# Optimization experiments

Measured on AMD Instinct MI355X. Metric: run time of the kernel, lower is better.

The kernel has to match this reference:

```python
import jax, jax.numpy as jnp
import numpy as np

ALPHA = 1.702  # gpt-oss gated-activation alpha
LIMIT = 7.0    # gpt-oss clamp limit
E, H, I = 8, 1024, 2048
B, S = 2, 2048


def setup_inputs() -> dict:
    key = jax.random.key(0)
    ks = jax.random.split(key, 6)
    return {
        "hidden_states": jax.random.normal(ks[0], (B, S, H), dtype=jnp.float32),
        "routing_weights": jax.random.uniform(ks[1], (B * S, E), dtype=jnp.float32),
        "gate_up_proj": jax.random.normal(ks[2], (E, H, 2 * I), dtype=jnp.float32) * 0.02,
        "gate_up_proj_bias": jax.random.normal(ks[3], (E, 2 * I), dtype=jnp.float32) * 0.02,
        "down_proj": jax.random.normal(ks[4], (E, I, H), dtype=jnp.float32) * 0.02,
        "down_proj_bias": jax.random.normal(ks[5], (E, H), dtype=jnp.float32) * 0.02,
    }


def reference(hidden_states, routing_weights, gate_up_proj, gate_up_proj_bias,
              down_proj, down_proj_bias):
    b, s, h = hidden_states.shape
    x = hidden_states.reshape(-1, h)  # [T, H]
    # all-experts dense path: [E, T, 2I]
    gate_up = jnp.einsum('th,ehd->etd', x, gate_up_proj) + gate_up_proj_bias[:, None, :]
    gate = gate_up[..., ::2]   # interleaved gate/up as in gpt-oss
    up = gate_up[..., 1::2]
    gate = jnp.minimum(gate, LIMIT)
    up = jnp.clip(up, -LIMIT, LIMIT)
    glu = gate * jax.nn.sigmoid(gate * ALPHA)
    # [E, T, H]
    out_e = jnp.einsum('eti,eih->eth', (up + 1.0) * glu, down_proj) + down_proj_bias[:, None, :]
    # weighted sum over experts with routing weights [T, E]
    out = jnp.einsum('eth,te->th', out_e, routing_weights)
    return out.reshape(b, s, h)
```

## Files before the change

### kernel.cpp

```cpp
#include <hip/hip_runtime.h>
#include <cstdint>

#define E_  8
#define H_  1024
#define I_  2048
#define T_  4096
#define D2_ 4096
#define K2_ 16384

typedef __bf16 bf16x8 __attribute__((ext_vector_type(8)));
typedef float  f32x4  __attribute__((ext_vector_type(4)));

__device__ __forceinline__ unsigned short f2bf(float f) {
  unsigned int u = __float_as_uint(f);
  u += 0x7FFFu + ((u >> 16) & 1u);
  return (unsigned short)(u >> 16);
}

__device__ __forceinline__ void gll16(const void* g, void* l) {
  __builtin_amdgcn_global_load_lds(
      (const __attribute__((address_space(1))) unsigned int*)(uintptr_t)g,
      (__attribute__((address_space(3))) unsigned int*)(uintptr_t)l,
      16, 0, 0);
}

#define BARX()  __builtin_amdgcn_s_barrier()
#define FENCE() __builtin_amdgcn_sched_barrier(0)
#define LGK0()  asm volatile("s_waitcnt lgkmcnt(0)" ::: "memory")
#define WVM0()  asm volatile("s_waitcnt vmcnt(0)" ::: "memory")

__global__ void cast_x_kernel(const float* __restrict__ x,
                              unsigned short* __restrict__ xb) {
  const int idx = (blockIdx.x * 256 + threadIdx.x) * 8;
  float4 a = *(const float4*)(x + idx);
  float4 b = *(const float4*)(x + idx + 4);
  unsigned short o[8];
  o[0]=f2bf(a.x); o[1]=f2bf(a.y); o[2]=f2bf(a.z); o[3]=f2bf(a.w);
  o[4]=f2bf(b.x); o[5]=f2bf(b.y); o[6]=f2bf(b.z); o[7]=f2bf(b.w);
  *(uint4*)(xb + idx) = *(const uint4*)o;
}

__global__ void transp_w1_kernel(const float* __restrict__ gup,
                                 unsigned short* __restrict__ w1g,
                                 unsigned short* __restrict__ w1u) {
  __shared__ float tile[64][65];
  const int h0 = blockIdx.x * 64;
  const int d0 = blockIdx.y * 64;
  const int e  = blockIdx.z;
  const int tid = threadIdx.x;
  const int r  = tid >> 4;
  const int c4 = (tid & 15) * 4;
  const float* src = gup + ((size_t)e * H_ + h0) * D2_ + d0;
#pragma unroll
  for (int c = 0; c < 4; ++c) {
    const int row = r + 16 * c;
    float4 v = *(const float4*)(src + (size_t)row * D2_ + c4);
    tile[row][c4+0] = v.x; tile[row][c4+1] = v.y;
    tile[row][c4+2] = v.z; tile[row][c4+3] = v.w;
  }
  __syncthreads();
  const int hl = tid & 63;
  const int jg = tid >> 6;
  const size_t jbase = (size_t)e * I_ + (d0 >> 1);
#pragma unroll
  for (int jj = 0; jj < 8; ++jj) {
    const int jl = jg * 8 + jj;
    w1g[(jbase + jl) * H_ + h0 + hl] = f2bf(tile[hl][2*jl]);
    w1u[(jbase + jl) * H_ + h0 + hl] = f2bf(tile[hl][2*jl+1]);
  }
}

__global__ void transp_w2_kernel(const float* __restrict__ dp,
                                 unsigned short* __restrict__ w2t) {
  __shared__ float tile[64][65];
  const int k0 = blockIdx.x * 64;
  const int h0 = blockIdx.y * 64;
  const int tid = threadIdx.x;
  const int r  = tid >> 4;
  const int c4 = (tid & 15) * 4;
#pragma unroll
  for (int c = 0; c < 4; ++c) {
    const int row = r + 16 * c;
    float4 v = *(const float4*)(dp + (size_t)(k0 + row) * H_ + h0 + c4);
    tile[row][c4+0] = v.x; tile[row][c4+1] = v.y;
    tile[row][c4+2] = v.z; tile[row][c4+3] = v.w;
  }
  __syncthreads();
  const int kl = tid & 63;
  const int hg = tid >> 6;
#pragma unroll
  for (int hh = 0; hh < 16; ++hh) {
    const int hl = hg * 16 + hh;
    w2t[(size_t)(h0 + hl) * K2_ + k0 + kl] = f2bf(tile[kl][hl]);
  }
}


#define NT1 32

#define STA1(B, KT) {                                                         \
  _Pragma("unroll")                                                           \
  for (int ld = 0; ld < 2; ++ld) {                                            \
    const int r = rS + ld*128;                                                \
    gll16(Ag + (size_t)r * H_ + (KT)*32 + sg, &lds[B][r*32 + sl]);            \
  }                                                                           \
  gll16(Gg + (size_t)rS * H_ + (KT)*32 + sg, &lds[B][8192  + rS*32 + sl]);    \
  gll16(Ug + (size_t)rS * H_ + (KT)*32 + sg, &lds[B][12288 + rS*32 + sl]);    \
}
#define LDALL1(B) {                                                           \
  _Pragma("unroll")                                                           \
  for (int m = 0; m < 8; ++m)                                                 \
    av[m] = *(const bf16x8*)&lds[B][(wm*128 + m*16 + arow)*32 + swr];         \
  _Pragma("unroll")                                                           \
  for (int n = 0; n < 2; ++n) {                                               \
    bgv[n] = *(const bf16x8*)&lds[B][8192  + (wn*32 + n*16 + arow)*32 + swr]; \
    buv[n] = *(const bf16x8*)&lds[B][12288 + (wn*32 + n*16 + arow)*32 + swr]; \
  } }
#define MMA1ALL() {                                                           \
  __builtin_amdgcn_s_setprio(1);                                              \
  _Pragma("unroll")                                                           \
  for (int m = 0; m < 8; ++m)                                                 \
  _Pragma("unroll")                                                           \
  for (int n = 0; n < 2; ++n) {                                               \
    accg[m][n] = __builtin_amdgcn_mfma_f32_16x16x32_bf16(av[m], bgv[n], accg[m][n], 0,0,0); \
    accu[m][n] = __builtin_amdgcn_mfma_f32_16x16x32_bf16(av[m], buv[n], accu[m][n], 0,0,0); \
  }                                                                           \
  __builtin_amdgcn_s_setprio(0); }

#define TILE1(B, U) {                                                         \
  if ((U)+1 < NT1) STA1((B)^1, (U)+1);                                        \
  FENCE();                                                                    \
  LDALL1(B);                                                                  \
  MMA1ALL();                                                                  \
  LGK0();                                                                     \
  if ((U)+1 < NT1) WVM0();                                                    \
  BARX();                                                                     \
  FENCE();                                                                    \
}

__global__ __launch_bounds__(512, 2) void gemm1_act_kernel(
    const unsigned short* __restrict__ xb,
    const unsigned short* __restrict__ w1g,
    const unsigned short* __restrict__ w1u,
    const float* __restrict__ gub,
    const float* __restrict__ rw,
    unsigned short* __restrict__ actW)
{
  __shared__ unsigned short lds[2][16384];
  const int tid  = threadIdx.x;
  const int lane = tid & 63;
  const int wv   = tid >> 6;
  const int wm   = wv >> 2;
  const int wn   = wv & 3;

  const int L  = blockIdx.x + 16 * blockIdx.y;
  const int xk = L & 7, xs = L >> 3;
  const int t0 = ((xk >> 1) * 4 + (xs & 3)) * 256;
  const int j0 = ((xk & 1) * 8 + (xs >> 2)) * 128;
  const int e  = blockIdx.z;

  const int arow = lane & 15;
  const int q    = lane >> 4;
  const int swr  = (q ^ ((arow >> 1) & 3)) * 8;
  const int sg   = ((tid & 3) ^ ((tid >> 3) & 3)) * 8;
  const int sl   = (tid & 3) * 8;
  const int rS   = tid >> 2;

  const unsigned short* Ag = xb  + (size_t)t0 * H_;
  const unsigned short* Gg = w1g + ((size_t)e * I_ + j0) * H_;
  const unsigned short* Ug = w1u + ((size_t)e * I_ + j0) * H_;

  const f32x4 zero = {0.f, 0.f, 0.f, 0.f};
  f32x4 accg[8][2], accu[8][2];
#pragma unroll
  for (int m = 0; m < 8; ++m)
#pragma unroll
    for (int n = 0; n < 2; ++n) { accg[m][n] = zero; accu[m][n] = zero; }
  bf16x8 av[8], bgv[2], buv[2];

  STA1(0, 0);
  WVM0(); BARX(); FENCE();

#pragma unroll 1
  for (int t = 0; t < NT1; t += 2) {
    TILE1(0, t);
    TILE1(1, t+1);
  }

  const float* gbE = gub + (size_t)e * D2_;
#pragma unroll
  for (int n = 0; n < 2; ++n) {
    const int j = j0 + wn*32 + n*16 + arow;
    const float2 bgu = *(const float2*)&gbE[2*j];
#pragma unroll
    for (int mf = 0; mf < 8; ++mf) {
#pragma unroll
      for (int ri = 0; ri < 4; ++ri) {
        const int t = t0 + wm*128 + mf*16 + q*4 + ri;
        float g = accg[mf][n][ri] + bgu.x;
        float u = accu[mf][n][ri] + bgu.y;
        g = fminf(g, 7.0f);
        u = fminf(fmaxf(u, -7.0f), 7.0f);
        const float s   = 1.0f / (1.0f + __expf(-1.702f * g));
        const float val = (u + 1.0f) * (g * s) * rw[t * 8 + e];
        actW[(size_t)t * K2_ + e * I_ + j] = f2bf(val);
      }
    }
  }
}


#define STA2(B, HF, KT) {                                                    \
  _Pragma("unroll")                                                           \
  for (int ld = 0; ld < 2; ++ld) {                                            \
    const int r = rA + (HF)*64 + ld*128;                                      \
    gll16(Ag + (size_t)r * K2_ + (KT)*64 + sg, &lds[B][r*64 + sl]);           \
  } }
#define STB2(B, NH, KT) {                                                    \
  _Pragma("unroll")                                                           \
  for (int ld = 0; ld < 2; ++ld) {                                            \
    const int lr = rA + ld*64;                                                \
    const int r  = (lr & 31) + (NH)*32 + ((lr >> 5) << 6);                    \
    gll16(Bgp + (size_t)r * K2_ + (KT)*64 + sg, &lds[B][16384 + r*64 + sl]);  \
  } }
#define LDA2(B, MH) {                                                         \
  _Pragma("unroll")                                                           \
  for (int m = 0; m < 4; ++m) {                                               \
    const int ro = (wm*128 + (MH)*64 + m*16 + arow) * 64;                     \
    av[m][0] = *(const bf16x8*)&lds[B][ro + sw0];                             \
    av[m][1] = *(const bf16x8*)&lds[B][ro + sw1];                             \
  } }
#define LDB2(B, DST, NH) {                                                   \
  _Pragma("unroll")                                                           \
  for (int n = 0; n < 2; ++n) {                                               \
    const int ro = 16384 + (wn*64 + (NH)*32 + n*16 + arow) * 64;              \
    DST[n][0] = *(const bf16x8*)&lds[B][ro + sw0];                            \
    DST[n][1] = *(const bf16x8*)&lds[B][ro + sw1];                            \
  } }
#define MMA2(MH, NH, BV)                                                      \
  __builtin_amdgcn_s_setprio(1);                                              \
  _Pragma("unroll")                                                           \
  for (int m = 0; m < 4; ++m)                                                 \
  _Pragma("unroll")                                                           \
  for (int n = 0; n < 2; ++n) {                                               \
    acc[(MH)*4+m][(NH)*2+n] = __builtin_amdgcn_mfma_f32_16x16x32_bf16(av[m][0], BV[n][0], acc[(MH)*4+m][(NH)*2+n], 0,0,0); \
    acc[(MH)*4+m][(NH)*2+n] = __builtin_amdgcn_mfma_f32_16x16x32_bf16(av[m][1], BV[n][1], acc[(MH)*4+m][(NH)*2+n], 0,0,0); \
  }                                                                           \
  __builtin_amdgcn_s_setprio(0);

#define NT2 64
#define TILE2(B, U) {                                                         \
  if ((U)+1 < NT2) { STA2((B)^1, 0, (U)+1); STA2((B)^1, 1, (U)+1);            \
                     STB2((B)^1, 0, (U)+1); STB2((B)^1, 1, (U)+1); }          \
  FENCE();                                                                    \
  LDA2(B, 0); LDB2(B, bv0, 0); LDB2(B, bv1, 1);                               \
  MMA2(0, 0, bv0); MMA2(0, 1, bv1);                                           \
  LDA2(B, 1);                                                                 \
  MMA2(1, 0, bv0); MMA2(1, 1, bv1);                                           \
  LGK0();                                                                     \
  if ((U)+1 < NT2) WVM0();                                                    \
  BARX();                                                                     \
  FENCE();                                                                    \
}

__global__ __launch_bounds__(512, 2) void gemm2_kernel(
    const unsigned short* __restrict__ actW,
    const unsigned short* __restrict__ w2t,
    float* __restrict__ part)
{
  __shared__ unsigned short lds[2][32768];
  const int tid  = threadIdx.x;
  const int lane = tid & 63;
  const int wv   = tid >> 6;
  const int wm   = wv >> 2;
  const int wn   = wv & 3;

  const int L  = blockIdx.x + 16 * (blockIdx.y + 4 * blockIdx.z);
  const int xk = L & 7, xs = L >> 3;
  const int t0 = ((xk & 1) * 8 + (xs & 7)) * 256;
  const int h0 = (xs >> 3) * 256;
  const int cz = xk >> 1;
  const int c0 = cz * 4096;

  const int arow = lane & 15;
  const int q    = lane >> 4;
  const int sw0  = ((q    ) ^ (arow & 7)) * 8;
  const int sw1  = ((q + 4) ^ (arow & 7)) * 8;
  const int sg   = ((tid & 7) ^ ((tid >> 3) & 7)) * 8;
  const int sl   = (tid & 7) * 8;
  const int rA   = tid >> 3;

  const unsigned short* Ag  = actW + (size_t)t0 * K2_ + c0;
  const unsigned short* Bgp = w2t  + (size_t)h0 * K2_ + c0;

  const f32x4 zero = {0.f, 0.f, 0.f, 0.f};
  f32x4 acc[8][4];
#pragma unroll
  for (int m = 0; m < 8; ++m)
#pragma unroll
    for (int n = 0; n < 4; ++n) acc[m][n] = zero;
  bf16x8 av[4][2], bv0[2][2], bv1[2][2];

  STA2(0, 0, 0); STA2(0, 1, 0); STB2(0, 0, 0); STB2(0, 1, 0);
  WVM0(); BARX(); FENCE();

#pragma unroll 1
  for (int t = 0; t < NT2; t += 2) {
    TILE2(0, t);
    TILE2(1, t+1);
  }

  float* P = part + (size_t)cz * ((size_t)T_ * H_);
#pragma unroll
  for (int mf = 0; mf < 8; ++mf)
#pragma unroll
    for (int nf = 0; nf < 4; ++nf)
#pragma unroll
      for (int ri = 0; ri < 4; ++ri) {
        const int t = t0 + wm*128 + mf*16 + q*4 + ri;
        const int h = h0 + wn*64 + nf*16 + arow;
        P[(size_t)t * H_ + h] = acc[mf][nf][ri];
      }
}

__global__ void reduce_kernel(const float* __restrict__ part,
                              const float* __restrict__ rw,
                              const float* __restrict__ dpb,
                              float* __restrict__ out) {
  const int idx = blockIdx.x * 256 + threadIdx.x;
  const int t  = idx >> 8;
  const int hq = idx & 255;
  const float4* p = (const float4*)part;
  float4 v = p[idx];
  float4 a;
  a = p[idx + 1048576]; v.x += a.x; v.y += a.y; v.z += a.z; v.w += a.w;
  a = p[idx + 2097152]; v.x += a.x; v.y += a.y; v.z += a.z; v.w += a.w;
  a = p[idx + 3145728]; v.x += a.x; v.y += a.y; v.z += a.z; v.w += a.w;
  const float4 w0 = *(const float4*)(rw + t*8);
  const float4 w1 = *(const float4*)(rw + t*8 + 4);
  const float wgt[8] = {w0.x, w0.y, w0.z, w0.w, w1.x, w1.y, w1.z, w1.w};
  const float4* db = (const float4*)dpb;
#pragma unroll
  for (int e2 = 0; e2 < 8; ++e2) {
    float4 b = db[e2*256 + hq];
    v.x += wgt[e2]*b.x; v.y += wgt[e2]*b.y; v.z += wgt[e2]*b.z; v.w += wgt[e2]*b.w;
  }
  ((float4*)out)[idx] = v;
}

extern "C" void kernel_launch(void* const* d_in, const int* in_sizes, int n_in,
                              void* d_out, int out_size, void* d_ws, size_t ws_size,
                              hipStream_t stream) {
  const float* hs  = (const float*)d_in[0];
  const float* rw  = (const float*)d_in[1];
  const float* gup = (const float*)d_in[2];
  const float* gub = (const float*)d_in[3];
  const float* dp  = (const float*)d_in[4];
  const float* dpb = (const float*)d_in[5];
  float* out = (float*)d_out;

  char* ws = (char*)d_ws;
  unsigned short* xb   = (unsigned short*)(ws);
  unsigned short* w1g  = (unsigned short*)(ws + 8388608);
  unsigned short* w1u  = (unsigned short*)(ws + 41943040);
  float*          part = (float*)(ws + 8388608);
  unsigned short* w2t  = (unsigned short*)(ws + 75497472);
  unsigned short* actW = (unsigned short*)(ws + 109051904);

  hipLaunchKernelGGL(cast_x_kernel, dim3((T_ * H_) / 2048), dim3(256), 0, stream, hs, xb);
  hipLaunchKernelGGL(transp_w1_kernel, dim3(H_/64, D2_/64, E_), dim3(256), 0, stream, gup, w1g, w1u);
  hipLaunchKernelGGL(transp_w2_kernel, dim3(K2_/64, H_/64), dim3(256), 0, stream, dp, w2t);
  hipLaunchKernelGGL(gemm1_act_kernel, dim3(T_/256, I_/128, E_), dim3(512), 0, stream,
                     xb, w1g, w1u, gub, rw, actW);
  hipLaunchKernelGGL(gemm2_kernel, dim3(T_/256, H_/256, 4), dim3(512), 0, stream,
                     actW, w2t, part);
  hipLaunchKernelGGL(reduce_kernel, dim3((T_ * H_ / 4) / 256), dim3(256), 0, stream,
                     part, rw, dpb, out);
}
```

Baseline: 470.6 us.

## Deepen both GEMM LDS pipelines to four stages with partial vmcnt waits

Both GEMM kernels now rotate through four LDS buffers, prefetching three K-tiles ahead. They replace the full vmcnt(0)/lgkmcnt(0) drain with partial vmcnt waits, and skip the trailing barrier on the last tile. This is meant to hide more global-load latency behind the MFMA work. GEMM2 also drops its K-tile from 64 to 32 so four stages fit in the same LDS footprint, reusing GEMM1's swizzle. GEMM1's LDS use doubles to 128 KB per block, which likely prevents two blocks per CU despite the launch bounds.

```diff
diff --git a/kernel.cpp b/kernel.cpp
--- a/kernel.cpp
+++ b/kernel.cpp
@@ -26,8 +26,9 @@
 
 #define BARX()  __builtin_amdgcn_s_barrier()
 #define FENCE() __builtin_amdgcn_sched_barrier(0)
-#define LGK0()  asm volatile("s_waitcnt lgkmcnt(0)" ::: "memory")
 #define WVM0()  asm volatile("s_waitcnt vmcnt(0)" ::: "memory")
+#define VM8()   asm volatile("s_waitcnt vmcnt(8)" ::: "memory")
+#define VM4()   asm volatile("s_waitcnt vmcnt(4)" ::: "memory")
 
 __global__ void cast_x_kernel(const float* __restrict__ x,
                               unsigned short* __restrict__ xb) {
@@ -98,7 +99,7 @@
 
 #define NT1 32
 
-#define STA1(B, KT) {                                                         \
+#define STG1ALL(B, KT) {                                                      \
   _Pragma("unroll")                                                           \
   for (int ld = 0; ld < 2; ++ld) {                                            \
     const int r = rS + ld*128;                                                \
@@ -128,14 +129,14 @@
   __builtin_amdgcn_s_setprio(0); }
 
 #define TILE1(B, U) {                                                         \
-  if ((U)+1 < NT1) STA1((B)^1, (U)+1);                                        \
+  if ((U)+3 < NT1) STG1ALL(((B)+3)&3, (U)+3);                                 \
   FENCE();                                                                    \
   LDALL1(B);                                                                  \
   MMA1ALL();                                                                  \
-  LGK0();                                                                     \
-  if ((U)+1 < NT1) WVM0();                                                    \
-  BARX();                                                                     \
-  FENCE();                                                                    \
+  if ((U)+3 < NT1)      { VM8(); }                                            \
+  else if ((U)+2 < NT1) { VM4(); }                                            \
+  else if ((U)+1 < NT1) { WVM0(); }                                           \
+  if ((U)+1 < NT1) { BARX(); FENCE(); }                                       \
 }
 
 __global__ __launch_bounds__(512, 2) void gemm1_act_kernel(
@@ -146,7 +147,7 @@
     const float* __restrict__ rw,
     unsigned short* __restrict__ actW)
 {
-  __shared__ unsigned short lds[2][16384];
+  __shared__ unsigned short lds[4][16384];
   const int tid  = threadIdx.x;
   const int lane = tid & 63;
   const int wv   = tid >> 6;
@@ -178,13 +179,15 @@
     for (int n = 0; n < 2; ++n) { accg[m][n] = zero; accu[m][n] = zero; }
   bf16x8 av[8], bgv[2], buv[2];
 
-  STA1(0, 0);
-  WVM0(); BARX(); FENCE();
+  STG1ALL(0, 0); STG1ALL(1, 1); STG1ALL(2, 2);
+  VM8(); BARX(); FENCE();
 
 #pragma unroll 1
-  for (int t = 0; t < NT1; t += 2) {
+  for (int t = 0; t < NT1; t += 4) {
     TILE1(0, t);
     TILE1(1, t+1);
+    TILE1(2, t+2);
+    TILE1(3, t+3);
   }
 
   const float* gbE = gub + (size_t)e * D2_;
@@ -210,57 +213,41 @@
 }
 
 
-#define STA2(B, HF, KT) {                                                    \
+#define NT2 128
+
+#define STG2ALL(B, KT) {                                                      \
   _Pragma("unroll")                                                           \
   for (int ld = 0; ld < 2; ++ld) {                                            \
-    const int r = rA + (HF)*64 + ld*128;                                      \
-    gll16(Ag + (size_t)r * K2_ + (KT)*64 + sg, &lds[B][r*64 + sl]);           \
+    const int r = rS + ld*128;                                                \
+    gll16(Ag  + (size_t)r * K2_ + (KT)*32 + sg, &lds[B][r*32 + sl]);          \
+    gll16(Bgp + (size_t)r * K2_ + (KT)*32 + sg, &lds[B][8192 + r*32 + sl]);   \
   } }
-#define STB2(B, NH, KT) {                                                    \
-  _Pragma("unroll")                                                           \
-  for (int ld = 0; ld < 2; ++ld) {                                            \
-    const int lr = rA + ld*64;                                                \
-    const int r  = (lr & 31) + (NH)*32 + ((lr >> 5) << 6);                    \
-    gll16(Bgp + (size_t)r * K2_ + (KT)*64 + sg, &lds[B][16384 + r*64 + sl]);  \
-  } }
-#define LDA2(B, MH) {                                                         \
-  _Pragma("unroll")                                                           \
-  for (int m = 0; m < 4; ++m) {                                               \
-    const int ro = (wm*128 + (MH)*64 + m*16 + arow) * 64;                     \
-    av[m][0] = *(const bf16x8*)&lds[B][ro + sw0];                             \
-    av[m][1] = *(const bf16x8*)&lds[B][ro + sw1];                             \
-  } }
-#define LDB2(B, DST, NH) {                                                   \
-  _Pragma("unroll")                                                           \
-  for (int n = 0; n < 2; ++n) {                                               \
-    const int ro = 16384 + (wn*64 + (NH)*32 + n*16 + arow) * 64;              \
-    DST[n][0] = *(const bf16x8*)&lds[B][ro + sw0];                            \
-    DST[n][1] = *(const bf16x8*)&lds[B][ro + sw1];                            \
-  } }
-#define MMA2(MH, NH, BV)                                                      \
+#define LDALL2(B) {                                                           \
+  _Pragma("unroll")                                                           \
+  for (int m = 0; m < 8; ++m)                                                 \
+    av[m] = *(const bf16x8*)&lds[B][(wm*128 + m*16 + arow)*32 + swr];         \
+  _Pragma("unroll")                                                           \
+  for (int n = 0; n < 4; ++n)                                                 \
+    bv[n] = *(const bf16x8*)&lds[B][8192 + (wn*64 + n*16 + arow)*32 + swr];   \
+}
+#define MMA2ALL() {                                                           \
   __builtin_amdgcn_s_setprio(1);                                              \
   _Pragma("unroll")                                                           \
-  for (int m = 0; m < 4; ++m)                                                 \
-  _Pragma("unroll")                                                           \
-  for (int n = 0; n < 2; ++n) {                                               \
-    acc[(MH)*4+m][(NH)*2+n] = __builtin_amdgcn_mfma_f32_16x16x32_bf16(av[m][0], BV[n][0], acc[(MH)*4+m][(NH)*2+n], 0,0,0); \
-    acc[(MH)*4+m][(NH)*2+n] = __builtin_amdgcn_mfma_f32_16x16x32_bf16(av[m][1], BV[n][1], acc[(MH)*4+m][(NH)*2+n], 0,0,0); \
-  }                                                                           \
-  __builtin_amdgcn_s_setprio(0);
-
-#define NT2 64
+  for (int m = 0; m < 8; ++m)                                                 \
+  _Pragma("unroll")                                                           \
+  for (int n = 0; n < 4; ++n)                                                 \
+    acc[m][n] = __builtin_amdgcn_mfma_f32_16x16x32_bf16(av[m], bv[n], acc[m][n], 0,0,0); \
+  __builtin_amdgcn_s_setprio(0); }
+
 #define TILE2(B, U) {                                                         \
-  if ((U)+1 < NT2) { STA2((B)^1, 0, (U)+1); STA2((B)^1, 1, (U)+1);            \
-                     STB2((B)^1, 0, (U)+1); STB2((B)^1, 1, (U)+1); }          \
+  if ((U)+3 < NT2) STG2ALL(((B)+3)&3, (U)+3);                                 \
   FENCE();                                                                    \
-  LDA2(B, 0); LDB2(B, bv0, 0); LDB2(B, bv1, 1);                               \
-  MMA2(0, 0, bv0); MMA2(0, 1, bv1);                                           \
-  LDA2(B, 1);                                                                 \
-  MMA2(1, 0, bv0); MMA2(1, 1, bv1);                                           \
-  LGK0();                                                                     \
-  if ((U)+1 < NT2) WVM0();                                                    \
-  BARX();                                                                     \
-  FENCE();                                                                    \
+  LDALL2(B);                                                                  \
+  MMA2ALL();                                                                  \
+  if ((U)+3 < NT2)      { VM8(); }                                            \
+  else if ((U)+2 < NT2) { VM4(); }                                            \
+  else if ((U)+1 < NT2) { WVM0(); }                                           \
+  if ((U)+1 < NT2) { BARX(); FENCE(); }                                       \
 }
 
 __global__ __launch_bounds__(512, 2) void gemm2_kernel(
@@ -268,7 +255,7 @@
     const unsigned short* __restrict__ w2t,
     float* __restrict__ part)
 {
-  __shared__ unsigned short lds[2][32768];
+  __shared__ unsigned short lds[4][16384];
   const int tid  = threadIdx.x;
   const int lane = tid & 63;
   const int wv   = tid >> 6;
@@ -284,11 +271,10 @@
 
   const int arow = lane & 15;
   const int q    = lane >> 4;
-  const int sw0  = ((q    ) ^ (arow & 7)) * 8;
-  const int sw1  = ((q + 4) ^ (arow & 7)) * 8;
-  const int sg   = ((tid & 7) ^ ((tid >> 3) & 7)) * 8;
-  const int sl   = (tid & 7) * 8;
-  const int rA   = tid >> 3;
+  const int swr  = (q ^ ((arow >> 1) & 3)) * 8;
+  const int sg   = ((tid & 3) ^ ((tid >> 3) & 3)) * 8;
+  const int sl   = (tid & 3) * 8;
+  const int rS   = tid >> 2;
 
   const unsigned short* Ag  = actW + (size_t)t0 * K2_ + c0;
   const unsigned short* Bgp = w2t  + (size_t)h0 * K2_ + c0;
@@ -299,15 +285,17 @@
   for (int m = 0; m < 8; ++m)
 #pragma unroll
     for (int n = 0; n < 4; ++n) acc[m][n] = zero;
-  bf16x8 av[4][2], bv0[2][2], bv1[2][2];
-
-  STA2(0, 0, 0); STA2(0, 1, 0); STB2(0, 0, 0); STB2(0, 1, 0);
-  WVM0(); BARX(); FENCE();
+  bf16x8 av[8], bv[4];
+
+  STG2ALL(0, 0); STG2ALL(1, 1); STG2ALL(2, 2);
+  VM8(); BARX(); FENCE();
 
 #pragma unroll 1
-  for (int t = 0; t < NT2; t += 2) {
+  for (int t = 0; t < NT2; t += 4) {
     TILE2(0, t);
     TILE2(1, t+1);
+    TILE2(2, t+2);
+    TILE2(3, t+3);
   }
 
   float* P = part + (size_t)cz * ((size_t)T_ * H_);
```

New measurement: 476.1 us. Within noise of the previous version (+1.2%).
